# Optimization experiments

Hardware: AMD Instinct MI355X
Metric: run time of the kernel (lower is better)

Reference implementation:

```python
import jax, jax.numpy as jnp
import numpy as np

N_NODES = 100000
N_EDGES = 1600000
IN_C, HID_C, OUT_C = 128, 128, 64


def gcn_conv(x, src, dst, W, b, num_nodes):
    # PyG GCNConv: add self-loops, symmetric normalization, linear transform,
    # aggregate source features into targets.
    h = x @ W  # [N, C_out]
    loop = jnp.arange(num_nodes, dtype=src.dtype)
    s = jnp.concatenate([src, loop])
    d = jnp.concatenate([dst, loop])
    deg = jax.ops.segment_sum(jnp.ones_like(d, dtype=h.dtype), d, num_segments=num_nodes)
    inv_sqrt = jnp.where(deg > 0, jax.lax.rsqrt(deg), 0.0)
    norm = inv_sqrt[s] * inv_sqrt[d]  # [E+N]
    msgs = h[s] * norm[:, None]  # gather + scale
    out = jax.ops.segment_sum(msgs, d, num_segments=num_nodes)  # scatter-add
    return out + b


def setup_inputs() -> dict:
    key = jax.random.key(0)
    k1, k2, k3, k4 = jax.random.split(key, 4)
    x = jax.random.normal(k1, (N_NODES, IN_C), dtype=jnp.float32)
    edge_index = jax.random.randint(k2, (2, N_EDGES), 0, N_NODES, dtype=jnp.int64)
    W1 = jax.random.normal(k3, (IN_C, HID_C), dtype=jnp.float32) * (1.0 / np.sqrt(IN_C))
    b1 = jnp.zeros((HID_C,), dtype=jnp.float32)
    W2 = jax.random.normal(k4, (HID_C, OUT_C), dtype=jnp.float32) * (1.0 / np.sqrt(HID_C))
    b2 = jnp.zeros((OUT_C,), dtype=jnp.float32)
    return {"x": x, "edge_index": edge_index, "W1": W1, "b1": b1, "W2": W2, "b2": b2}


def reference(x, edge_index, W1, b1, W2, b2):
    num_nodes = x.shape[0]
    src, dst = edge_index[0], edge_index[1]  # PyG flow: source -> target
    h = gcn_conv(x, src, dst, W1, b1, num_nodes)
    h = jax.nn.relu(h)  # dropout is identity in eval mode
    out = gcn_conv(h, src, dst, W2, b2, num_nodes)
    return out
```

## Files before the change

kernel.cpp:

```cpp
#include <hip/hip_runtime.h>

#define IN_C 128
#define HID_C 128
#define OUT_C 64

#define BSPAN 256
#define BCAP  5120
#define NBMAX 512
#define ACHUNK 4096

typedef unsigned int uint32;
typedef unsigned short ushort16;
typedef _Float16 f16;
typedef f16   f16x8 __attribute__((ext_vector_type(8)));
typedef float f32x4 __attribute__((ext_vector_type(4)));


__device__ __forceinline__ ushort16 f2bf(float f) {
    union { float f; uint32 u; } v; v.f = f;
    uint32 r = v.u + 0x7FFFu + ((v.u >> 16) & 1u);
    return (ushort16)(r >> 16);
}

__device__ __forceinline__ void unpack2(uint32 u, float& f0, float& f1) {
    union { uint32 x; float f; } a, b;
    a.x = u << 16;
    b.x = u & 0xFFFF0000u;
    f0 = a.f; f1 = b.f;
}

__device__ __forceinline__ void acc_row(uint4 r, float* acc) {
    float f0, f1;
    unpack2(r.x, f0, f1); acc[0] += f0; acc[1] += f1;
    unpack2(r.y, f0, f1); acc[2] += f0; acc[3] += f1;
    unpack2(r.z, f0, f1); acc[4] += f0; acc[5] += f1;
    unpack2(r.w, f0, f1); acc[6] += f0; acc[7] += f1;
}

template <int C>
__device__ __forceinline__ void wprep_one(const float* __restrict__ W, f16* __restrict__ Wf, int t) {
    constexpr int NCT = C / 16;
    int lane = t & 63;
    int ctkc = t >> 6;
    int ct = ctkc % NCT, kc = ctkc / NCT;
    int kbase = kc * 32 + (lane >> 4) * 8;
    int col   = ct * 16 + (lane & 15);
    f16 v[8];
#pragma unroll
    for (int j = 0; j < 8; j++) v[j] = (f16)W[(size_t)(kbase + j) * C + col];
    *(uint4*)(Wf + (size_t)t * 8) = *(const uint4*)v;
}


__launch_bounds__(256)
__global__ void k1_bin_wprep(const int* __restrict__ src, const int* __restrict__ dst,
                             int* __restrict__ bucketCur, int* __restrict__ deg,
                             uint32* __restrict__ binned,
                             const float* __restrict__ W1, f16* __restrict__ Wf1,
                             const float* __restrict__ W2, f16* __restrict__ Wf2,
                             int E, int nbuck, int nchunk) {
    const int tid = threadIdx.x;
    if ((int)blockIdx.x >= nchunk) {
        int t = ((int)blockIdx.x - nchunk) * 256 + tid;
        constexpr int T1 = 4 * (HID_C / 16) * 64;
        constexpr int T2 = 4 * (OUT_C / 16) * 64;
        if (t < T1)           wprep_one<HID_C>(W1, Wf1, t);
        else if (t < T1 + T2) wprep_one<OUT_C>(W2, Wf2, t - T1);
        return;
    }
    __shared__ int hist[NBMAX];
    __shared__ int base[NBMAX];
    const int e0 = blockIdx.x * ACHUNK;

    for (int i = tid; i < NBMAX; i += 256) hist[i] = 0;
    __syncthreads();

    int d[16], s[16], rk[16];
#pragma unroll
    for (int j = 0; j < 16; j++) {
        int e = e0 + j * 256 + tid;
        if (e < E) {
            d[j] = dst[e];
            s[j] = src[e];
            rk[j] = atomicAdd(&hist[d[j] >> 8], 1);
            atomicAdd(&deg[d[j]], 1);
        } else d[j] = -1;
    }
    __syncthreads();

    for (int b = tid; b < nbuck; b += 256) {
        int h = hist[b];
        base[b] = h ? atomicAdd(&bucketCur[b], h) : 0;
    }
    __syncthreads();

#pragma unroll
    for (int j = 0; j < 16; j++) {
        if (d[j] >= 0) {
            int b = d[j] >> 8;
            int pos = base[b] + rk[j];
            if (pos < BCAP)
                binned[(size_t)b * BCAP + pos] =
                    ((uint32)(d[j] & 255) << 17) | (uint32)s[j];
        }
    }
}


__launch_bounds__(256)
__global__ void k2_csr_gemm1(const uint32* __restrict__ binned, const int* __restrict__ bucketCur,
                             const int* __restrict__ deg,
                             int* __restrict__ csrs, int* __restrict__ rowbeg,
                             int* __restrict__ rowend, float* __restrict__ inv,
                             const float* __restrict__ x, const f16* __restrict__ Wf1,
                             ushort16* __restrict__ hs1b, int N, int nbuck) {
    __shared__ __align__(16) f16 As[4 * 4 * 64 * 8];
    const int tid = threadIdx.x;

    if ((int)blockIdx.x < nbuck) {
        int* cnt = (int*)As;
        int* scn = cnt + BSPAN;
        int* ex  = scn + BSPAN;
        const int b  = blockIdx.x;
        const int ne = min(bucketCur[b], BCAP);
        const uint32* bp = binned + (size_t)b * BCAP;

        cnt[tid] = 0;
        __syncthreads();

        int rbuf[BCAP / 256];
        int nm = 0;
        for (int i = tid; i < ne; i += 256)
            rbuf[nm++] = atomicAdd(&cnt[bp[i] >> 17], 1);
        __syncthreads();

        int v = cnt[tid];
        scn[tid] = v;
        __syncthreads();
        for (int off = 1; off < 256; off <<= 1) {
            int u = (tid >= off) ? scn[tid - off] : 0;
            __syncthreads();
            scn[tid] += u;
            __syncthreads();
        }
        int e0 = scn[tid] - v;
        ex[tid] = e0;

        int n = b * BSPAN + tid;
        if (n < N) {
            int gb = b * BCAP + e0;
            rowbeg[n] = gb;
            rowend[n] = gb + v;
            inv[n] = rsqrtf((float)(v + 1));
        }
        __syncthreads();

        nm = 0;
        for (int i = tid; i < ne; i += 256) {
            uint32 e = bp[i];
            csrs[(size_t)b * BCAP + ex[e >> 17] + rbuf[nm++]] = (int)(e & 0x1FFFFu);
        }
        return;
    }

    const int lane = tid & 63;
    const int w    = tid >> 6;
    const int row0 = ((int)blockIdx.x - nbuck) * 64;

    {
        int r   = tid >> 2;
        int seg = tid & 3;
        int row = row0 + r;
        int ws_ = r >> 4;
        int r15 = r & 15;
#pragma unroll
        for (int i = 0; i < 8; i++) {
            int k = seg * 32 + i * 4;
            float4 v = make_float4(0.f, 0.f, 0.f, 0.f);
            if (row < N) v = *(const float4*)(x + (size_t)row * 128 + k);
            int q = (k >> 3) & 3, j0 = k & 7;
            f16 h[4] = {(f16)v.x, (f16)v.y, (f16)v.z, (f16)v.w};
            int slot = ((seg * 4 + ws_) * 64 + (q * 16 + r15)) * 8 + j0;
            *(uint2*)(As + slot) = *(const uint2*)h;
        }
    }
    __syncthreads();

    f32x4 acc[8];
#pragma unroll
    for (int c = 0; c < 8; c++) acc[c] = (f32x4){0.f, 0.f, 0.f, 0.f};
#pragma unroll
    for (int kc = 0; kc < 4; kc++) {
        f16x8 a = *(const f16x8*)&As[((kc * 4 + w) * 64 + lane) * 8];
#pragma unroll
        for (int ct = 0; ct < 8; ct++) {
            f16x8 b = *(const f16x8*)&Wf1[(size_t)(((kc * 8 + ct) * 64) + lane) * 8];
            acc[ct] = __builtin_amdgcn_mfma_f32_16x16x32_f16(a, b, acc[ct], 0, 0, 0);
        }
    }

    __syncthreads();
    ushort16* Ds = (ushort16*)As;
    const int q = lane >> 4;
    float iv[4];
#pragma unroll
    for (int reg = 0; reg < 4; reg++) {
        int row = row0 + w * 16 + q * 4 + reg;
        iv[reg] = (row < N) ? rsqrtf((float)(deg[row] + 1)) : 0.f;
    }
#pragma unroll
    for (int ct = 0; ct < 8; ct++)
#pragma unroll
        for (int reg = 0; reg < 4; reg++) {
            int r = w * 16 + q * 4 + reg;
            Ds[r * 128 + ct * 16 + (lane & 15)] = f2bf(acc[ct][reg] * iv[reg]);
        }
    __syncthreads();
    {
        int r   = tid >> 2;
        int row = row0 + r;
        if (row < N) {
            int c0 = (tid & 3) * 32;
            const uint4* s = (const uint4*)&Ds[r * 128 + c0];
            uint4* d = (uint4*)(hs1b + (size_t)row * 128 + c0);
#pragma unroll
            for (int i = 0; i < 4; i++) d[i] = s[i];
        }
    }
}


__launch_bounds__(256)
__global__ void k3_fused(const int* __restrict__ rowbeg, const int* __restrict__ rowend,
                         const int* __restrict__ csrs,
                         const ushort16* __restrict__ hs1b, const float* __restrict__ inv,
                         const float* __restrict__ b1, const f16* __restrict__ Wf2,
                         ushort16* __restrict__ hs2b, int N) {
    constexpr int NCT = OUT_C / 16;
    __shared__ __align__(16) f16 As[4 * 4 * 64 * 8];

    const int tid  = threadIdx.x;
    const int lane = tid & 63;
    const int w    = tid >> 6;
    const int row0 = blockIdx.x * 64;

    {
        int r = tid >> 2;
        int q = tid & 3;
        int n = row0 + r;
        float acc[32];
#pragma unroll
        for (int j = 0; j < 32; j++) acc[j] = 0.f;

        if (n < N) {
            const ushort16* base = hs1b + (size_t)n * 128 + q * 32;
            uint4 s0 = *(const uint4*)(base);
            uint4 s1 = *(const uint4*)(base + 8);
            uint4 s2 = *(const uint4*)(base + 16);
            uint4 s3 = *(const uint4*)(base + 24);
            acc_row(s0, acc); acc_row(s1, acc + 8);
            acc_row(s2, acc + 16); acc_row(s3, acc + 24);

            int beg = rowbeg[n], end = rowend[n];
            int i = beg;
            for (; i + 2 <= end; i += 2) {
                const ushort16* p0 = hs1b + (size_t)csrs[i]     * 128 + q * 32;
                const ushort16* p1 = hs1b + (size_t)csrs[i + 1] * 128 + q * 32;
                uint4 a0 = *(const uint4*)(p0);
                uint4 a1 = *(const uint4*)(p0 + 8);
                uint4 a2 = *(const uint4*)(p0 + 16);
                uint4 a3 = *(const uint4*)(p0 + 24);
                uint4 c0 = *(const uint4*)(p1);
                uint4 c1 = *(const uint4*)(p1 + 8);
                uint4 c2 = *(const uint4*)(p1 + 16);
                uint4 c3 = *(const uint4*)(p1 + 24);
                acc_row(a0, acc);      acc_row(a1, acc + 8);
                acc_row(a2, acc + 16); acc_row(a3, acc + 24);
                acc_row(c0, acc);      acc_row(c1, acc + 8);
                acc_row(c2, acc + 16); acc_row(c3, acc + 24);
            }
            if (i < end) {
                const ushort16* p0 = hs1b + (size_t)csrs[i] * 128 + q * 32;
                uint4 a0 = *(const uint4*)(p0);
                uint4 a1 = *(const uint4*)(p0 + 8);
                uint4 a2 = *(const uint4*)(p0 + 16);
                uint4 a3 = *(const uint4*)(p0 + 24);
                acc_row(a0, acc);      acc_row(a1, acc + 8);
                acc_row(a2, acc + 16); acc_row(a3, acc + 24);
            }

            float ivn = inv[n];
#pragma unroll
            for (int j = 0; j < 32; j++)
                acc[j] = fmaxf(fmaf(ivn, acc[j], b1[q * 32 + j]), 0.f);
        }

        int ws_ = r >> 4, r15 = r & 15;
#pragma unroll
        for (int i8 = 0; i8 < 4; i8++) {
            f16 h[8];
#pragma unroll
            for (int j = 0; j < 8; j++) h[j] = (f16)acc[i8 * 8 + j];
            int slot = ((q * 4 + ws_) * 64 + (i8 * 16 + r15)) * 8;
            *(uint4*)(As + slot) = *(const uint4*)h;
        }
    }
    __syncthreads();

    f32x4 acc2[NCT];
#pragma unroll
    for (int c = 0; c < NCT; c++) acc2[c] = (f32x4){0.f, 0.f, 0.f, 0.f};
#pragma unroll
    for (int kc = 0; kc < 4; kc++) {
        f16x8 a = *(const f16x8*)&As[((kc * 4 + w) * 64 + lane) * 8];
#pragma unroll
        for (int ct = 0; ct < NCT; ct++) {
            f16x8 b = *(const f16x8*)&Wf2[(size_t)(((kc * NCT + ct) * 64) + lane) * 8];
            acc2[ct] = __builtin_amdgcn_mfma_f32_16x16x32_f16(a, b, acc2[ct], 0, 0, 0);
        }
    }

    __syncthreads();
    ushort16* Ds = (ushort16*)As;
    const int q2 = lane >> 4;
    float iv2[4];
#pragma unroll
    for (int reg = 0; reg < 4; reg++) {
        int row = row0 + w * 16 + q2 * 4 + reg;
        iv2[reg] = (row < N) ? inv[row] : 0.f;
    }
#pragma unroll
    for (int ct = 0; ct < NCT; ct++)
#pragma unroll
        for (int reg = 0; reg < 4; reg++) {
            int r = w * 16 + q2 * 4 + reg;
            Ds[r * 64 + ct * 16 + (lane & 15)] = f2bf(acc2[ct][reg] * iv2[reg]);
        }
    __syncthreads();
    {
        int r   = tid >> 2;
        int row = row0 + r;
        if (row < N) {
            int c0 = (tid & 3) * 16;
            const uint4* s = (const uint4*)&Ds[r * 64 + c0];
            uint4* d = (uint4*)(hs2b + (size_t)row * 64 + c0);
#pragma unroll
            for (int i = 0; i < 2; i++) d[i] = s[i];
        }
    }
}


template <int C, bool RELU>
__launch_bounds__(256)
__global__ void gather_agg_bf16(const int* __restrict__ rowbeg, const int* __restrict__ rowend,
                                const int* __restrict__ csr_src,
                                const ushort16* __restrict__ hsb, const float* __restrict__ inv,
                                const float* __restrict__ b, float* __restrict__ out, int N) {
    constexpr int TPN = C / 8;
    constexpr int NPB = 256 / TPN;
    int n    = blockIdx.x * NPB + threadIdx.x / TPN;
    int lane = threadIdx.x % TPN;
    if (n >= N) return;
    int c8 = lane * 8;

    float acc[8];
    {
        uint4 raw = *(const uint4*)(hsb + (size_t)n * C + c8);
        unpack2(raw.x, acc[0], acc[1]);
        unpack2(raw.y, acc[2], acc[3]);
        unpack2(raw.z, acc[4], acc[5]);
        unpack2(raw.w, acc[6], acc[7]);
    }

    int beg = rowbeg[n];
    int end = rowend[n];
    int i = beg;
    for (; i + 4 <= end; i += 4) {
        int s0 = csr_src[i];
        int s1 = csr_src[i + 1];
        int s2 = csr_src[i + 2];
        int s3 = csr_src[i + 3];
        uint4 r0 = *(const uint4*)(hsb + (size_t)s0 * C + c8);
        uint4 r1 = *(const uint4*)(hsb + (size_t)s1 * C + c8);
        uint4 r2 = *(const uint4*)(hsb + (size_t)s2 * C + c8);
        uint4 r3 = *(const uint4*)(hsb + (size_t)s3 * C + c8);
        acc_row(r0, acc); acc_row(r1, acc); acc_row(r2, acc); acc_row(r3, acc);
    }
    for (; i < end; i++) {
        uint4 r0 = *(const uint4*)(hsb + (size_t)csr_src[i] * C + c8);
        acc_row(r0, acc);
    }

    float iv = inv[n];
    float4 b0 = *(const float4*)(b + c8);
    float4 b1 = *(const float4*)(b + c8 + 4);
    float r[8];
    r[0] = fmaf(iv, acc[0], b0.x); r[1] = fmaf(iv, acc[1], b0.y);
    r[2] = fmaf(iv, acc[2], b0.z); r[3] = fmaf(iv, acc[3], b0.w);
    r[4] = fmaf(iv, acc[4], b1.x); r[5] = fmaf(iv, acc[5], b1.y);
    r[6] = fmaf(iv, acc[6], b1.z); r[7] = fmaf(iv, acc[7], b1.w);
    if (RELU) {
#pragma unroll
        for (int j = 0; j < 8; j++) r[j] = fmaxf(r[j], 0.f);
    }
    float* po = out + (size_t)n * C + c8;
    *(float4*)(po)     = make_float4(r[0], r[1], r[2], r[3]);
    *(float4*)(po + 4) = make_float4(r[4], r[5], r[6], r[7]);
}

extern "C" void kernel_launch(void* const* d_in, const int* in_sizes, int n_in,
                              void* d_out, int out_size, void* d_ws, size_t ws_size,
                              hipStream_t stream) {
    const float* x  = (const float*)d_in[0];
    const int*   ei = (const int*)d_in[1];
    const float* W1 = (const float*)d_in[2];
    const float* b1 = (const float*)d_in[3];
    const float* W2 = (const float*)d_in[4];
    const float* b2 = (const float*)d_in[5];
    float* out = (float*)d_out;

    const int N = in_sizes[0] / IN_C;
    const int E = in_sizes[1] / 2;
    const int* src = ei;
    const int* dst = ei + E;
    const int nbuck  = (N + BSPAN - 1) / BSPAN;
    const int nchunk = (E + ACHUNK - 1) / ACHUNK;
    const int ntile  = (N + 63) / 64;
    const int wpb    = (4 * (HID_C/16 + OUT_C/16) * 64 + 255) / 256;

    char* ws = (char*)d_ws;
    auto align_up = [](size_t v) { return (v + 1023) & ~(size_t)1023; };
    size_t off = 0;
    int*      deg       = (int*)(ws + off);      off += (size_t)N * sizeof(int);
    int*      bucketCur = (int*)(ws + off);      off += align_up((size_t)nbuck * sizeof(int));
    size_t    zbytes    = off;
    float*    inv       = (float*)(ws + off);    off += align_up((size_t)N * sizeof(float));
    int*      rowbeg    = (int*)(ws + off);      off += align_up((size_t)N * sizeof(int));
    int*      rowend    = (int*)(ws + off);      off += align_up((size_t)N * sizeof(int));
    uint32*   binned    = (uint32*)(ws + off);   off += align_up((size_t)nbuck * BCAP * sizeof(uint32));
    int*      csrs      = (int*)(ws + off);      off += align_up((size_t)nbuck * BCAP * sizeof(int));
    f16*      Wf1       = (f16*)(ws + off);      off += align_up((size_t)4 * (HID_C/16) * 64 * 8 * sizeof(f16));
    f16*      Wf2       = (f16*)(ws + off);      off += align_up((size_t)4 * (OUT_C/16) * 64 * 8 * sizeof(f16));
    ushort16* hs1b      = (ushort16*)(ws + off); off += align_up((size_t)N * HID_C * sizeof(ushort16));
    ushort16* hs2b      = (ushort16*)(ws + off); off += align_up((size_t)N * OUT_C * sizeof(ushort16));

    hipMemsetAsync(deg, 0, zbytes, stream);

    k1_bin_wprep<<<nchunk + wpb, 256, 0, stream>>>(
        src, dst, bucketCur, deg, binned, W1, Wf1, W2, Wf2, E, nbuck, nchunk);

    k2_csr_gemm1<<<nbuck + ntile, 256, 0, stream>>>(
        binned, bucketCur, deg, csrs, rowbeg, rowend, inv, x, Wf1, hs1b, N, nbuck);

    k3_fused<<<ntile, 256, 0, stream>>>(
        rowbeg, rowend, csrs, hs1b, inv, b1, Wf2, hs2b, N);

    {
        constexpr int NPB = 256 / (OUT_C / 8);
        gather_agg_bf16<OUT_C, false><<<(N + NPB - 1) / NPB, 256, 0, stream>>>(
            rowbeg, rowend, csrs, hs2b, inv, b2, out, N);
    }
}
```

Measured before the change: 316.7 us.

## Drop global degree atomics, split bucket-CSR and GEMM1 kernels, halve edge chunk

Removes the per-edge global atomicAdd on the degree array in the binning kernel. Degree is now taken from the per-bucket CSR count (inv), which means GEMM1 must run after CSR construction, so the fused CSR+GEMM kernel is split into two launches. The edge chunk per block is halved to raise parallelism in binning. This trades global atomic traffic and the larger memset for one extra kernel launch and the loss of overlap between CSR building and GEMM1.

```diff
diff --git a/kernel.cpp b/kernel.cpp
--- a/kernel.cpp
+++ b/kernel.cpp
@@ -7,7 +7,7 @@
 #define BSPAN 256
 #define BCAP  5120
 #define NBMAX 512
-#define ACHUNK 4096
+#define ACHUNK 2048
 
 typedef unsigned int uint32;
 typedef unsigned short ushort16;
@@ -54,8 +54,7 @@
 
 __launch_bounds__(256)
 __global__ void k1_bin_wprep(const int* __restrict__ src, const int* __restrict__ dst,
-                             int* __restrict__ bucketCur, int* __restrict__ deg,
-                             uint32* __restrict__ binned,
+                             int* __restrict__ bucketCur, uint32* __restrict__ binned,
                              const float* __restrict__ W1, f16* __restrict__ Wf1,
                              const float* __restrict__ W2, f16* __restrict__ Wf2,
                              int E, int nbuck, int nchunk) {
@@ -75,15 +74,14 @@
     for (int i = tid; i < NBMAX; i += 256) hist[i] = 0;
     __syncthreads();
 
-    int d[16], s[16], rk[16];
-#pragma unroll
-    for (int j = 0; j < 16; j++) {
+    int d[8], s[8], rk[8];
+#pragma unroll
+    for (int j = 0; j < 8; j++) {
         int e = e0 + j * 256 + tid;
         if (e < E) {
             d[j] = dst[e];
             s[j] = src[e];
             rk[j] = atomicAdd(&hist[d[j] >> 8], 1);
-            atomicAdd(&deg[d[j]], 1);
         } else d[j] = -1;
     }
     __syncthreads();
@@ -95,7 +93,7 @@
     __syncthreads();
 
 #pragma unroll
-    for (int j = 0; j < 16; j++) {
+    for (int j = 0; j < 8; j++) {
         if (d[j] >= 0) {
             int b = d[j] >> 8;
             int pos = base[b] + rk[j];
@@ -108,64 +106,63 @@
 
 
 __launch_bounds__(256)
-__global__ void k2_csr_gemm1(const uint32* __restrict__ binned, const int* __restrict__ bucketCur,
-                             const int* __restrict__ deg,
-                             int* __restrict__ csrs, int* __restrict__ rowbeg,
-                             int* __restrict__ rowend, float* __restrict__ inv,
-                             const float* __restrict__ x, const f16* __restrict__ Wf1,
-                             ushort16* __restrict__ hs1b, int N, int nbuck) {
+__global__ void k2_bucket_csr(const uint32* __restrict__ binned, const int* __restrict__ bucketCur,
+                              int* __restrict__ csrs, int* __restrict__ rowbeg,
+                              int* __restrict__ rowend, float* __restrict__ inv, int N) {
+    __shared__ int cnt[BSPAN];
+    __shared__ int scn[BSPAN];
+    __shared__ int ex[BSPAN];
+    const int b   = blockIdx.x;
+    const int tid = threadIdx.x;
+    const int ne  = min(bucketCur[b], BCAP);
+    const uint32* bp = binned + (size_t)b * BCAP;
+
+    cnt[tid] = 0;
+    __syncthreads();
+
+    int rbuf[BCAP / 256];
+    int nm = 0;
+    for (int i = tid; i < ne; i += 256)
+        rbuf[nm++] = atomicAdd(&cnt[bp[i] >> 17], 1);
+    __syncthreads();
+
+    int v = cnt[tid];
+    scn[tid] = v;
+    __syncthreads();
+    for (int off = 1; off < 256; off <<= 1) {
+        int u = (tid >= off) ? scn[tid - off] : 0;
+        __syncthreads();
+        scn[tid] += u;
+        __syncthreads();
+    }
+    int e0 = scn[tid] - v;
+    ex[tid] = e0;
+
+    int n = b * BSPAN + tid;
+    if (n < N) {
+        int gb = b * BCAP + e0;
+        rowbeg[n] = gb;
+        rowend[n] = gb + v;
+        inv[n] = rsqrtf((float)(v + 1));
+    }
+    __syncthreads();
+
+    nm = 0;
+    for (int i = tid; i < ne; i += 256) {
+        uint32 e = bp[i];
+        csrs[(size_t)b * BCAP + ex[e >> 17] + rbuf[nm++]] = (int)(e & 0x1FFFFu);
+    }
+}
+
+
+__launch_bounds__(256)
+__global__ void k3_gemm1(const float* __restrict__ x, const f16* __restrict__ Wf1,
+                         const float* __restrict__ inv, ushort16* __restrict__ hs1b, int N) {
     __shared__ __align__(16) f16 As[4 * 4 * 64 * 8];
-    const int tid = threadIdx.x;
-
-    if ((int)blockIdx.x < nbuck) {
-        int* cnt = (int*)As;
-        int* scn = cnt + BSPAN;
-        int* ex  = scn + BSPAN;
-        const int b  = blockIdx.x;
-        const int ne = min(bucketCur[b], BCAP);
-        const uint32* bp = binned + (size_t)b * BCAP;
-
-        cnt[tid] = 0;
-        __syncthreads();
-
-        int rbuf[BCAP / 256];
-        int nm = 0;
-        for (int i = tid; i < ne; i += 256)
-            rbuf[nm++] = atomicAdd(&cnt[bp[i] >> 17], 1);
-        __syncthreads();
-
-        int v = cnt[tid];
-        scn[tid] = v;
-        __syncthreads();
-        for (int off = 1; off < 256; off <<= 1) {
-            int u = (tid >= off) ? scn[tid - off] : 0;
-            __syncthreads();
-            scn[tid] += u;
-            __syncthreads();
-        }
-        int e0 = scn[tid] - v;
-        ex[tid] = e0;
-
-        int n = b * BSPAN + tid;
-        if (n < N) {
-            int gb = b * BCAP + e0;
-            rowbeg[n] = gb;
-            rowend[n] = gb + v;
-            inv[n] = rsqrtf((float)(v + 1));
-        }
-        __syncthreads();
-
-        nm = 0;
-        for (int i = tid; i < ne; i += 256) {
-            uint32 e = bp[i];
-            csrs[(size_t)b * BCAP + ex[e >> 17] + rbuf[nm++]] = (int)(e & 0x1FFFFu);
-        }
-        return;
-    }
-
+    const int tid  = threadIdx.x;
     const int lane = tid & 63;
     const int w    = tid >> 6;
-    const int row0 = ((int)blockIdx.x - nbuck) * 64;
+    const int row0 = blockIdx.x * 64;
 
     {
         int r   = tid >> 2;
@@ -206,7 +203,7 @@
 #pragma unroll
     for (int reg = 0; reg < 4; reg++) {
         int row = row0 + w * 16 + q * 4 + reg;
-        iv[reg] = (row < N) ? rsqrtf((float)(deg[row] + 1)) : 0.f;
+        iv[reg] = (row < N) ? inv[row] : 0.f;
     }
 #pragma unroll
     for (int ct = 0; ct < 8; ct++)
@@ -231,7 +228,7 @@
 
 
 __launch_bounds__(256)
-__global__ void k3_fused(const int* __restrict__ rowbeg, const int* __restrict__ rowend,
+__global__ void k4_fused(const int* __restrict__ rowbeg, const int* __restrict__ rowend,
                          const int* __restrict__ csrs,
                          const ushort16* __restrict__ hs1b, const float* __restrict__ inv,
                          const float* __restrict__ b1, const f16* __restrict__ Wf2,
@@ -432,9 +429,7 @@
     char* ws = (char*)d_ws;
     auto align_up = [](size_t v) { return (v + 1023) & ~(size_t)1023; };
     size_t off = 0;
-    int*      deg       = (int*)(ws + off);      off += (size_t)N * sizeof(int);
     int*      bucketCur = (int*)(ws + off);      off += align_up((size_t)nbuck * sizeof(int));
-    size_t    zbytes    = off;
     float*    inv       = (float*)(ws + off);    off += align_up((size_t)N * sizeof(float));
     int*      rowbeg    = (int*)(ws + off);      off += align_up((size_t)N * sizeof(int));
     int*      rowend    = (int*)(ws + off);      off += align_up((size_t)N * sizeof(int));
@@ -445,15 +440,17 @@
     ushort16* hs1b      = (ushort16*)(ws + off); off += align_up((size_t)N * HID_C * sizeof(ushort16));
     ushort16* hs2b      = (ushort16*)(ws + off); off += align_up((size_t)N * OUT_C * sizeof(ushort16));
 
-    hipMemsetAsync(deg, 0, zbytes, stream);
+    hipMemsetAsync(bucketCur, 0, (size_t)nbuck * sizeof(int), stream);
 
     k1_bin_wprep<<<nchunk + wpb, 256, 0, stream>>>(
-        src, dst, bucketCur, deg, binned, W1, Wf1, W2, Wf2, E, nbuck, nchunk);
-
-    k2_csr_gemm1<<<nbuck + ntile, 256, 0, stream>>>(
-        binned, bucketCur, deg, csrs, rowbeg, rowend, inv, x, Wf1, hs1b, N, nbuck);
-
-    k3_fused<<<ntile, 256, 0, stream>>>(
+        src, dst, bucketCur, binned, W1, Wf1, W2, Wf2, E, nbuck, nchunk);
+
+    k2_bucket_csr<<<nbuck, 256, 0, stream>>>(
+        binned, bucketCur, csrs, rowbeg, rowend, inv, N);
+
+    k3_gemm1<<<ntile, 256, 0, stream>>>(x, Wf1, inv, hs1b, N);
+
+    k4_fused<<<ntile, 256, 0, stream>>>(
         rowbeg, rowend, csrs, hs1b, inv, b1, Wf2, hs2b, N);
 
     {
```

Measured after the change: 279.9 us. 11.6% less time.
